# Optimization experiments

Hardware: AMD Instinct MI355X
Metric: run time of the kernel (lower is better)

The kernel has to match this reference:

```python
import jax, jax.numpy as jnp
import numpy as np

H = 32        # num query heads
HKV = 8       # num kv heads
D = 128       # head_dim
SCALE = D ** -0.5
FP8_MAX = 448.0   # e4m3 max
EPS = 1e-8
PAGE = 256
NPAGES = 20
SQ = 1024     # new diffusion tokens
CTX = 3072    # cached context tokens
DIFF_BLK = 32 # diffusion block size


def setup_inputs() -> dict:
    key = jax.random.key(0)
    ks = jax.random.split(key, 6)
    q = jax.random.normal(ks[0], (SQ, H * D), dtype=jnp.float32)
    k = jax.random.normal(ks[1], (SQ, HKV * D), dtype=jnp.float32)
    v = jax.random.normal(ks[2], (SQ, HKV * D), dtype=jnp.float32)
    # paged caches (values already stored in quantized units)
    k_cache = jax.random.normal(ks[3], (NPAGES, PAGE, HKV, D), dtype=jnp.float32)
    v_cache = jax.random.normal(ks[4], (NPAGES, PAGE, HKV, D), dtype=jnp.float32)
    # new tokens go into slots right after the context
    slot_mapping = jnp.arange(CTX, CTX + SQ, dtype=jnp.int32)
    cache_slots = jnp.arange(CTX, dtype=jnp.int32)
    # diffusion mask: full visibility of context, block-causal among new tokens
    blk = jnp.arange(SQ) // DIFF_BLK
    ctx_mask = jnp.ones((SQ, CTX), dtype=bool)
    new_mask = blk[:, None] >= blk[None, :]
    block_mask = jnp.concatenate([ctx_mask, new_mask], axis=1)  # [SQ, CTX+SQ]
    return {"q": q, "k": k, "v": v, "k_cache": k_cache, "v_cache": v_cache,
            "slot_mapping": slot_mapping, "cache_slots": cache_slots,
            "block_mask": block_mask}


def reference(q, k, v, k_cache, v_cache, slot_mapping, cache_slots, block_mask):
    k3 = k.reshape(-1, HKV, D)
    v3 = v.reshape(-1, HKV, D)
    qh = q.reshape(-1, H, D)

    # ---- FP8 scale tracking: per-kv-head absmax over (token, dim) ----
    k_scale = jnp.maximum(jnp.max(jnp.abs(k3), axis=(0, 2)) / FP8_MAX, EPS)  # [HKV]
    v_scale = jnp.maximum(jnp.max(jnp.abs(v3), axis=(0, 2)) / FP8_MAX, EPS)

    # ---- paged KV-cache store with inline quantization ----
    kc = k_cache.reshape(-1, HKV, D)  # [NPAGES*PAGE, HKV, D]
    vc = v_cache.reshape(-1, HKV, D)
    k_q = jnp.clip(k3 / k_scale[None, :, None], -FP8_MAX, FP8_MAX)
    v_q = jnp.clip(v3 / v_scale[None, :, None], -FP8_MAX, FP8_MAX)
    kc = kc.at[slot_mapping].set(k_q)
    vc = vc.at[slot_mapping].set(v_q)

    # ---- load context tokens from cache and dequantize ----
    k_ctx = kc[cache_slots] * k_scale[None, :, None]  # [CTX, HKV, D]
    v_ctx = vc[cache_slots] * v_scale[None, :, None]
    k_comb = jnp.concatenate([k_ctx, k3], axis=0)  # [SKV, HKV, D]
    v_comb = jnp.concatenate([v_ctx, v3], axis=0)

    # ---- GQA flex attention with token-level block mask ----
    G = H // HKV
    k_g = jnp.repeat(k_comb, G, axis=1)  # [SKV, H, D]
    v_g = jnp.repeat(v_comb, G, axis=1)
    scores = jnp.einsum('qhd,khd->hqk', qh, k_g) * SCALE  # [H, SQ, SKV]
    scores = jnp.where(block_mask[None, :, :], scores, jnp.float32(-1e30))
    probs = jax.nn.softmax(scores, axis=-1)
    o = jnp.einsum('hqk,khd->qhd', probs, v_g)  # [SQ, H, D]
    return o.reshape(-1, H * D)
```

## Files before the change

kernel.cpp:

```cpp
#include <hip/hip_runtime.h>
#include <stdint.h>

#define H 32
#define HKV 8
#define D 128
#define SQ 1024
#define CTX 3072
#define SKV 4096
#define FP8_MAX_C 448.0f
#define EPS_C 1e-8f

typedef __attribute__((ext_vector_type(4))) float f32x4;
typedef __attribute__((ext_vector_type(8))) __bf16 bf16x8;
typedef __attribute__((ext_vector_type(8))) unsigned short u16x8;
typedef __attribute__((ext_vector_type(4))) unsigned short u16x4;

__device__ __forceinline__ unsigned short f2bf(float x) {
  unsigned int u = __builtin_bit_cast(unsigned int, x);
  u += 0x7fffu + ((u >> 16) & 1u);
  return (unsigned short)(u >> 16);
}

__device__ __forceinline__ f32x4 mfma16(bf16x8 a, bf16x8 b, f32x4 c) {
  return __builtin_amdgcn_mfma_f32_16x16x32_bf16(a, b, c, 0, 0, 0);
}

__device__ __forceinline__ void gld16(const unsigned short* g, char* l) {
  __builtin_amdgcn_global_load_lds(
      (const __attribute__((address_space(1))) unsigned int*)g,
      (__attribute__((address_space(3))) unsigned int*)l, 16, 0, 0);
}

__device__ __forceinline__ void stage_sync() {
  asm volatile("s_waitcnt vmcnt(0)" ::: "memory");
  __builtin_amdgcn_sched_barrier(0);
  __syncthreads();
}

__global__ void scales_part(const float* __restrict__ k,
                            const float* __restrict__ v,
                            unsigned int* __restrict__ smax) {
  const int b = blockIdx.x & 15;
  const int part = blockIdx.x >> 4;
  const float* src = (b < HKV) ? k : v;
  const int h = b & 7;
  const int tid = threadIdx.x;
  const int d0 = (tid & 31) * 4;
  float mx = 0.f;
  const int t1 = part * 128 + 128;
  for (int t = part * 128 + (tid >> 5); t < t1; t += 8) {
    float4 vv = *reinterpret_cast<const float4*>(src + (size_t)t * (HKV * D) + h * D + d0);
    mx = fmaxf(mx, fmaxf(fmaxf(fabsf(vv.x), fabsf(vv.y)),
                         fmaxf(fabsf(vv.z), fabsf(vv.w))));
  }
  __shared__ float red[256];
  red[tid] = mx;
  __syncthreads();
  for (int s = 128; s > 0; s >>= 1) {
    if (tid < s) red[tid] = fmaxf(red[tid], red[tid + s]);
    __syncthreads();
  }
  if (tid == 0) atomicMax(&smax[b], __float_as_uint(red[0]));
}

__global__ void scales_fin(const unsigned int* __restrict__ smax,
                           float* __restrict__ scales) {
  const int i = threadIdx.x;
  if (i < 16) scales[i] = fmaxf(__uint_as_float(smax[i]) / FP8_MAX_C, EPS_C);
}

__global__ void prep_k(const float* __restrict__ k,
                       const float* __restrict__ k_cache,
                       const int* __restrict__ cache_slots,
                       const float* __restrict__ scales,
                       unsigned short* __restrict__ k_comb) {
  const int tid = blockIdx.x * 256 + threadIdx.x;
  const int d8 = tid & 15;
  const int t = (tid >> 4) & (SKV - 1);
  const int h = tid >> 16;
  const int d0 = d8 * 8;
  const float* src;
  float mul;
  if (t < CTX) {
    int slot = cache_slots[t];
    src = k_cache + (size_t)slot * (HKV * D) + h * D + d0;
    mul = scales[h];
  } else {
    src = k + (size_t)(t - CTX) * (HKV * D) + h * D + d0;
    mul = 1.f;
  }
  float4 a = *reinterpret_cast<const float4*>(src);
  float4 bb = *reinterpret_cast<const float4*>(src + 4);
  u16x8 r;
  r[0] = f2bf(a.x * mul);  r[1] = f2bf(a.y * mul);
  r[2] = f2bf(a.z * mul);  r[3] = f2bf(a.w * mul);
  r[4] = f2bf(bb.x * mul); r[5] = f2bf(bb.y * mul);
  r[6] = f2bf(bb.z * mul); r[7] = f2bf(bb.w * mul);
  *reinterpret_cast<u16x8*>(k_comb + ((size_t)h * SKV + t) * D + d0) = r;
}

__global__ void prep_v(const float* __restrict__ v,
                       const float* __restrict__ v_cache,
                       const int* __restrict__ cache_slots,
                       const float* __restrict__ scales,
                       unsigned short* __restrict__ v_combT) {
  const int tid = blockIdx.x * 256 + threadIdx.x;
  const int d = tid & 127;
  const int t8 = (tid >> 7) & 511;
  const int h = tid >> 16;
  const int t0 = t8 * 8;
  const float sc = scales[8 + h];
  u16x8 r;
#pragma unroll
  for (int i = 0; i < 8; ++i) {
    int t = t0 + i;
    float val;
    if (t < CTX) {
      int slot = cache_slots[t];
      val = v_cache[(size_t)slot * (HKV * D) + h * D + d] * sc;
    } else {
      val = v[(size_t)(t - CTX) * (HKV * D) + h * D + d];
    }
    r[i] = f2bf(val);
  }
  *reinterpret_cast<u16x8*>(v_combT + ((size_t)h * D + d) * SKV + t0) = r;
}

#define LDBF(p) (*reinterpret_cast<const bf16x8*>(p))
#define Z4 ((f32x4){0.f, 0.f, 0.f, 0.f})

#define STAGE(TB, BUFO)                                                        \
  {                                                                            \
    _Pragma("unroll")                                                          \
    for (int j = 0; j < 4; ++j) {                                              \
      const int c = wid * 256 + j * 64 + l;                                    \
      const int r_ = c >> 4;                                                   \
      const int lc_ = (c & 15) ^ (r_ & 7);                                     \
      gld16(kb + (size_t)((TB) + r_) * D + lc_ * 8,                            \
            smem + (BUFO) + (wid * 256 + j * 64) * 16);                        \
      const int dv_ = c >> 3;                                                  \
      const int lv_ = (c & 7) ^ (dv_ & 7);                                     \
      gld16(vb + (size_t)dv_ * SKV + (TB) + lv_ * 8,                           \
            smem + (BUFO) + 16384 + (wid * 256 + j * 64) * 16);                \
    }                                                                          \
  }

#define PK(SREG, PKREG)                                                        \
  {                                                                            \
    float p0_ = __builtin_amdgcn_exp2f(SREG[0] - m);                           \
    float p1_ = __builtin_amdgcn_exp2f(SREG[1] - m);                           \
    float p2_ = __builtin_amdgcn_exp2f(SREG[2] - m);                           \
    float p3_ = __builtin_amdgcn_exp2f(SREG[3] - m);                           \
    rs += (p0_ + p1_) + (p2_ + p3_);                                           \
    PKREG[0] = f2bf(p0_); PKREG[1] = f2bf(p1_);                                \
    PKREG[2] = f2bf(p2_); PKREG[3] = f2bf(p3_);                                \
  }

__launch_bounds__(256, 2)
__global__ void attn_kernel(const float* __restrict__ q,
                            const unsigned short* __restrict__ k_comb,
                            const unsigned short* __restrict__ v_combT,
                            float* __restrict__ out) {
  extern __shared__ __align__(16) char smem[];
  const int bid = blockIdx.x;
  const int hkv = bid & 7;
  const int qt = bid >> 3;
  const int wid = threadIdx.x >> 6;
  const int l = threadIdx.x & 63;
  const int lo = l & 15;
  const int g = l >> 4;
  const int hq = hkv * 4 + wid;
  const int qbase = qt * 16;
  const int nt32 = 97 + (qt >> 1);
  const int n64 = (nt32 + 1) >> 1;
  const bool odd = (nt32 & 1) != 0;

  const unsigned short* kb = k_comb + (size_t)hkv * SKV * D;
  const unsigned short* vb = v_combT + (size_t)hkv * D * SKV;

  bf16x8 qf0, qf1, qf2, qf3;
  {
    const float qs = 0.088388347648318447f * 1.4426950408889634f;
    const float* qp = q + (size_t)(qbase + lo) * (H * D) + hq * D;
#define QLOAD(KS, DST)                                                         \
    {                                                                          \
      float4 a = *reinterpret_cast<const float4*>(qp + KS * 32 + g * 8);       \
      float4 b = *reinterpret_cast<const float4*>(qp + KS * 32 + g * 8 + 4);   \
      union { unsigned short u[8]; bf16x8 v; } f;                              \
      f.u[0] = f2bf(a.x * qs); f.u[1] = f2bf(a.y * qs);                        \
      f.u[2] = f2bf(a.z * qs); f.u[3] = f2bf(a.w * qs);                        \
      f.u[4] = f2bf(b.x * qs); f.u[5] = f2bf(b.y * qs);                        \
      f.u[6] = f2bf(b.z * qs); f.u[7] = f2bf(b.w * qs);                        \
      DST = f.v;                                                               \
    }
    QLOAD(0, qf0) QLOAD(1, qf1) QLOAD(2, qf2) QLOAD(3, qf3)
#undef QLOAD
  }

  f32x4 acc0 = Z4, acc1 = Z4, acc2 = Z4, acc3 = Z4;
  f32x4 acc4 = Z4, acc5 = Z4, acc6 = Z4, acc7 = Z4;
  float m = -1e30f;
  float lsum = 0.f;

  const int xr = lo & 7;
  const int kx0 = ((0 + g) ^ xr) << 4;
  const int kx1 = ((4 + g) ^ xr) << 4;
  const int kx2 = ((8 + g) ^ xr) << 4;
  const int kx3 = ((12 + g) ^ xr) << 4;
  const int vxa = ((g) ^ xr) << 4;
  const int vxb = ((g + 4) ^ xr) << 4;
  const char* kbl = smem + lo * 256;
  const char* vbl = smem + 16384 + lo * 128;
  unsigned short* p_lds = (unsigned short*)(smem + 65536);
  unsigned short* prow = p_lds + (wid * 16 + lo) * 72;

  int cur = 0;
  STAGE(0, 0)
  stage_sync();

  for (int t = 0; t < n64; ++t) {
    const int tb = t * 64;
    if (t + 1 < n64) STAGE(tb + 64, (cur ^ 1) * 32768)

    const char* kc = kbl + cur * 32768;
    const char* vc = vbl + cur * 32768;

    f32x4 s0 = Z4, s1 = Z4, s2 = Z4, s3 = Z4;
    {
      bf16x8 a0 = LDBF(kc + 0 * 4096 + kx0);
      bf16x8 a1 = LDBF(kc + 0 * 4096 + kx1);
      bf16x8 a2 = LDBF(kc + 0 * 4096 + kx2);
      bf16x8 a3 = LDBF(kc + 0 * 4096 + kx3);
      s0 = mfma16(a0, qf0, s0); s0 = mfma16(a1, qf1, s0);
      s0 = mfma16(a2, qf2, s0); s0 = mfma16(a3, qf3, s0);
    }
    {
      bf16x8 a0 = LDBF(kc + 1 * 4096 + kx0);
      bf16x8 a1 = LDBF(kc + 1 * 4096 + kx1);
      bf16x8 a2 = LDBF(kc + 1 * 4096 + kx2);
      bf16x8 a3 = LDBF(kc + 1 * 4096 + kx3);
      s1 = mfma16(a0, qf0, s1); s1 = mfma16(a1, qf1, s1);
      s1 = mfma16(a2, qf2, s1); s1 = mfma16(a3, qf3, s1);
    }
    {
      bf16x8 a0 = LDBF(kc + 2 * 4096 + kx0);
      bf16x8 a1 = LDBF(kc + 2 * 4096 + kx1);
      bf16x8 a2 = LDBF(kc + 2 * 4096 + kx2);
      bf16x8 a3 = LDBF(kc + 2 * 4096 + kx3);
      s2 = mfma16(a0, qf0, s2); s2 = mfma16(a1, qf1, s2);
      s2 = mfma16(a2, qf2, s2); s2 = mfma16(a3, qf3, s2);
    }
    {
      bf16x8 a0 = LDBF(kc + 3 * 4096 + kx0);
      bf16x8 a1 = LDBF(kc + 3 * 4096 + kx1);
      bf16x8 a2 = LDBF(kc + 3 * 4096 + kx2);
      bf16x8 a3 = LDBF(kc + 3 * 4096 + kx3);
      s3 = mfma16(a0, qf0, s3); s3 = mfma16(a1, qf1, s3);
      s3 = mfma16(a2, qf2, s3); s3 = mfma16(a3, qf3, s3);
    }

    if (odd && t == n64 - 1) {
      s2 = (f32x4){-1e30f, -1e30f, -1e30f, -1e30f};
      s3 = (f32x4){-1e30f, -1e30f, -1e30f, -1e30f};
    }

    float pmax = fmaxf(fmaxf(fmaxf(s0[0], s0[1]), fmaxf(s0[2], s0[3])),
                       fmaxf(fmaxf(s1[0], s1[1]), fmaxf(s1[2], s1[3])));
    pmax = fmaxf(pmax,
                 fmaxf(fmaxf(fmaxf(s2[0], s2[1]), fmaxf(s2[2], s2[3])),
                       fmaxf(fmaxf(s3[0], s3[1]), fmaxf(s3[2], s3[3]))));
    if (!__all(pmax - m <= 8.f)) {
      float rm = fmaxf(pmax, __shfl_xor(pmax, 16));
      rm = fmaxf(rm, __shfl_xor(rm, 32));
      float mn = fmaxf(m, rm);
      float scl = __builtin_amdgcn_exp2f(m - mn);
      lsum *= scl;
      acc0 *= scl; acc1 *= scl; acc2 *= scl; acc3 *= scl;
      acc4 *= scl; acc5 *= scl; acc6 *= scl; acc7 *= scl;
      m = mn;
    }

    float rs = 0.f;
    u16x4 pk0, pk1, pk2, pk3;
    PK(s0, pk0) PK(s1, pk1) PK(s2, pk2) PK(s3, pk3)
    lsum += rs;

    *reinterpret_cast<u16x4*>(prow + 0 * 16 + g * 4) = pk0;
    *reinterpret_cast<u16x4*>(prow + 1 * 16 + g * 4) = pk1;
    *reinterpret_cast<u16x4*>(prow + 2 * 16 + g * 4) = pk2;
    *reinterpret_cast<u16x4*>(prow + 3 * 16 + g * 4) = pk3;
    bf16x8 pf0 = LDBF(prow + g * 8);
    bf16x8 pf1 = LDBF(prow + 32 + g * 8);

    {
      bf16x8 va = LDBF(vc + 0 * 2048 + vxa), vb_ = LDBF(vc + 0 * 2048 + vxb);
      acc0 = mfma16(pf0, va, acc0); acc0 = mfma16(pf1, vb_, acc0);
    }
    {
      bf16x8 va = LDBF(vc + 1 * 2048 + vxa), vb_ = LDBF(vc + 1 * 2048 + vxb);
      acc1 = mfma16(pf0, va, acc1); acc1 = mfma16(pf1, vb_, acc1);
    }
    {
      bf16x8 va = LDBF(vc + 2 * 2048 + vxa), vb_ = LDBF(vc + 2 * 2048 + vxb);
      acc2 = mfma16(pf0, va, acc2); acc2 = mfma16(pf1, vb_, acc2);
    }
    {
      bf16x8 va = LDBF(vc + 3 * 2048 + vxa), vb_ = LDBF(vc + 3 * 2048 + vxb);
      acc3 = mfma16(pf0, va, acc3); acc3 = mfma16(pf1, vb_, acc3);
    }
    {
      bf16x8 va = LDBF(vc + 4 * 2048 + vxa), vb_ = LDBF(vc + 4 * 2048 + vxb);
      acc4 = mfma16(pf0, va, acc4); acc4 = mfma16(pf1, vb_, acc4);
    }
    {
      bf16x8 va = LDBF(vc + 5 * 2048 + vxa), vb_ = LDBF(vc + 5 * 2048 + vxb);
      acc5 = mfma16(pf0, va, acc5); acc5 = mfma16(pf1, vb_, acc5);
    }
    {
      bf16x8 va = LDBF(vc + 6 * 2048 + vxa), vb_ = LDBF(vc + 6 * 2048 + vxb);
      acc6 = mfma16(pf0, va, acc6); acc6 = mfma16(pf1, vb_, acc6);
    }
    {
      bf16x8 va = LDBF(vc + 7 * 2048 + vxa), vb_ = LDBF(vc + 7 * 2048 + vxb);
      acc7 = mfma16(pf0, va, acc7); acc7 = mfma16(pf1, vb_, acc7);
    }

    stage_sync();
    cur ^= 1;
  }

  lsum += __shfl_xor(lsum, 16);
  lsum += __shfl_xor(lsum, 32);
#pragma unroll
  for (int r = 0; r < 4; ++r) {
    int src = (l & 48) | (g * 4 + r);
    float inv = 1.f / __shfl(lsum, src);
    float* op = out + (size_t)(qbase + g * 4 + r) * (H * D) + hq * D + lo;
    op[0 * 16] = acc0[r] * inv;
    op[1 * 16] = acc1[r] * inv;
    op[2 * 16] = acc2[r] * inv;
    op[3 * 16] = acc3[r] * inv;
    op[4 * 16] = acc4[r] * inv;
    op[5 * 16] = acc5[r] * inv;
    op[6 * 16] = acc6[r] * inv;
    op[7 * 16] = acc7[r] * inv;
  }
}

extern "C" void kernel_launch(void* const* d_in, const int* in_sizes, int n_in,
                              void* d_out, int out_size, void* d_ws, size_t ws_size,
                              hipStream_t stream) {
  (void)in_sizes; (void)n_in; (void)out_size; (void)ws_size;
  const float* q = (const float*)d_in[0];
  const float* k = (const float*)d_in[1];
  const float* v = (const float*)d_in[2];
  const float* k_cache = (const float*)d_in[3];
  const float* v_cache = (const float*)d_in[4];
  const int* cache_slots = (const int*)d_in[6];
  float* out = (float*)d_out;

  unsigned int* smax = (unsigned int*)d_ws;
  float* scales = (float*)((char*)d_ws + 64);
  unsigned short* k_comb = (unsigned short*)((char*)d_ws + 256);
  unsigned short* v_combT = k_comb + (size_t)HKV * SKV * D;

  hipMemsetAsync(smax, 0, 64, stream);
  scales_part<<<128, 256, 0, stream>>>(k, v, smax);
  scales_fin<<<1, 64, 0, stream>>>(smax, scales);
  prep_k<<<2048, 256, 0, stream>>>(k, k_cache, cache_slots, scales, k_comb);
  prep_v<<<2048, 256, 0, stream>>>(v, v_cache, cache_slots, scales, v_combT);
  attn_kernel<<<512, 256, 74752, stream>>>(q, k_comb, v_combT, out);
}
```

Measured before the change: 133.6 us.

## Process two query heads per wave to reuse K/V LDS fragments

Each wave now computes attention for two query heads of the same KV group instead of one, so every K and V fragment read from LDS feeds two MFMAs. The block shrinks from 4 waves to 2, and the staging loop is reorganised so 128 threads fill the same shared K/V tiles. The two heads share one running max, which must be taken over both heads' scores. This cuts LDS reads per MFMA but doubles accumulator registers and halves the waves available for latency hiding per CU.

Result: slower. 168.3 us (+26.0%).

```diff
diff --git a/kernel.cpp b/kernel.cpp
--- a/kernel.cpp
+++ b/kernel.cpp
@@ -132,31 +132,51 @@
 #define STAGE(TB, BUFO)                                                        \
   {                                                                            \
     _Pragma("unroll")                                                          \
-    for (int j = 0; j < 4; ++j) {                                              \
-      const int c = wid * 256 + j * 64 + l;                                    \
+    for (int j = 0; j < 8; ++j) {                                              \
+      const int c = j * 128 + tid;                                             \
       const int r_ = c >> 4;                                                   \
       const int lc_ = (c & 15) ^ (r_ & 7);                                     \
       gld16(kb + (size_t)((TB) + r_) * D + lc_ * 8,                            \
-            smem + (BUFO) + (wid * 256 + j * 64) * 16);                        \
+            smem + (BUFO) + c * 16);                                           \
       const int dv_ = c >> 3;                                                  \
       const int lv_ = (c & 7) ^ (dv_ & 7);                                     \
       gld16(vb + (size_t)dv_ * SKV + (TB) + lv_ * 8,                           \
-            smem + (BUFO) + 16384 + (wid * 256 + j * 64) * 16);                \
+            smem + (BUFO) + 16384 + c * 16);                                   \
     }                                                                          \
   }
 
-#define PK(SREG, PKREG)                                                        \
+#define PK(SREG, PKREG, RSV)                                                   \
   {                                                                            \
     float p0_ = __builtin_amdgcn_exp2f(SREG[0] - m);                           \
     float p1_ = __builtin_amdgcn_exp2f(SREG[1] - m);                           \
     float p2_ = __builtin_amdgcn_exp2f(SREG[2] - m);                           \
     float p3_ = __builtin_amdgcn_exp2f(SREG[3] - m);                           \
-    rs += (p0_ + p1_) + (p2_ + p3_);                                           \
+    RSV += (p0_ + p1_) + (p2_ + p3_);                                          \
     PKREG[0] = f2bf(p0_); PKREG[1] = f2bf(p1_);                                \
     PKREG[2] = f2bf(p2_); PKREG[3] = f2bf(p3_);                                \
   }
 
-__launch_bounds__(256, 2)
+#define QKSF(SF, SA, SB)                                                       \
+  {                                                                            \
+    bf16x8 a0 = LDBF(kc + SF * 4096 + kx0);                                    \
+    bf16x8 a1 = LDBF(kc + SF * 4096 + kx1);                                    \
+    bf16x8 a2 = LDBF(kc + SF * 4096 + kx2);                                    \
+    bf16x8 a3 = LDBF(kc + SF * 4096 + kx3);                                    \
+    SA = mfma16(a0, qa0, SA); SA = mfma16(a1, qa1, SA);                        \
+    SA = mfma16(a2, qa2, SA); SA = mfma16(a3, qa3, SA);                        \
+    SB = mfma16(a0, qb0, SB); SB = mfma16(a1, qb1, SB);                        \
+    SB = mfma16(a2, qb2, SB); SB = mfma16(a3, qb3, SB);                        \
+  }
+
+#define PVDT(DT, AA, AB)                                                       \
+  {                                                                            \
+    bf16x8 va = LDBF(vc + DT * 2048 + vxa);                                    \
+    bf16x8 vw = LDBF(vc + DT * 2048 + vxb);                                    \
+    AA = mfma16(pfa0, va, AA); AA = mfma16(pfa1, vw, AA);                      \
+    AB = mfma16(pfb0, va, AB); AB = mfma16(pfb1, vw, AB);                      \
+  }
+
+__launch_bounds__(128, 1)
 __global__ void attn_kernel(const float* __restrict__ q,
                             const unsigned short* __restrict__ k_comb,
                             const unsigned short* __restrict__ v_combT,
@@ -165,11 +185,12 @@
   const int bid = blockIdx.x;
   const int hkv = bid & 7;
   const int qt = bid >> 3;
-  const int wid = threadIdx.x >> 6;
-  const int l = threadIdx.x & 63;
+  const int tid = threadIdx.x;
+  const int wid = tid >> 6;
+  const int l = tid & 63;
   const int lo = l & 15;
   const int g = l >> 4;
-  const int hq = hkv * 4 + wid;
+  const int hqa = hkv * 4 + wid * 2;
   const int qbase = qt * 16;
   const int nt32 = 97 + (qt >> 1);
   const int n64 = (nt32 + 1) >> 1;
@@ -178,14 +199,14 @@
   const unsigned short* kb = k_comb + (size_t)hkv * SKV * D;
   const unsigned short* vb = v_combT + (size_t)hkv * D * SKV;
 
-  bf16x8 qf0, qf1, qf2, qf3;
+  bf16x8 qa0, qa1, qa2, qa3, qb0, qb1, qb2, qb3;
   {
     const float qs = 0.088388347648318447f * 1.4426950408889634f;
-    const float* qp = q + (size_t)(qbase + lo) * (H * D) + hq * D;
-#define QLOAD(KS, DST)                                                         \
+    const float* qpA = q + (size_t)(qbase + lo) * (H * D) + hqa * D;
+#define QLOAD(PTR, KS, DST)                                                    \
     {                                                                          \
-      float4 a = *reinterpret_cast<const float4*>(qp + KS * 32 + g * 8);       \
-      float4 b = *reinterpret_cast<const float4*>(qp + KS * 32 + g * 8 + 4);   \
+      float4 a = *reinterpret_cast<const float4*>((PTR) + KS * 32 + g * 8);    \
+      float4 b = *reinterpret_cast<const float4*>((PTR) + KS * 32 + g * 8 + 4);\
       union { unsigned short u[8]; bf16x8 v; } f;                              \
       f.u[0] = f2bf(a.x * qs); f.u[1] = f2bf(a.y * qs);                        \
       f.u[2] = f2bf(a.z * qs); f.u[3] = f2bf(a.w * qs);                        \
@@ -193,14 +214,18 @@
       f.u[6] = f2bf(b.z * qs); f.u[7] = f2bf(b.w * qs);                        \
       DST = f.v;                                                               \
     }
-    QLOAD(0, qf0) QLOAD(1, qf1) QLOAD(2, qf2) QLOAD(3, qf3)
+    QLOAD(qpA, 0, qa0) QLOAD(qpA, 1, qa1) QLOAD(qpA, 2, qa2) QLOAD(qpA, 3, qa3)
+    const float* qpB = qpA + D;
+    QLOAD(qpB, 0, qb0) QLOAD(qpB, 1, qb1) QLOAD(qpB, 2, qb2) QLOAD(qpB, 3, qb3)
 #undef QLOAD
   }
 
-  f32x4 acc0 = Z4, acc1 = Z4, acc2 = Z4, acc3 = Z4;
-  f32x4 acc4 = Z4, acc5 = Z4, acc6 = Z4, acc7 = Z4;
+  f32x4 aa0 = Z4, aa1 = Z4, aa2 = Z4, aa3 = Z4;
+  f32x4 aa4 = Z4, aa5 = Z4, aa6 = Z4, aa7 = Z4;
+  f32x4 ab0 = Z4, ab1 = Z4, ab2 = Z4, ab3 = Z4;
+  f32x4 ab4 = Z4, ab5 = Z4, ab6 = Z4, ab7 = Z4;
   float m = -1e30f;
-  float lsum = 0.f;
+  float lsa = 0.f, lsb = 0.f;
 
   const int xr = lo & 7;
   const int kx0 = ((0 + g) ^ xr) << 4;
@@ -211,8 +236,8 @@
   const int vxb = ((g + 4) ^ xr) << 4;
   const char* kbl = smem + lo * 256;
   const char* vbl = smem + 16384 + lo * 128;
-  unsigned short* p_lds = (unsigned short*)(smem + 65536);
-  unsigned short* prow = p_lds + (wid * 16 + lo) * 72;
+  unsigned short* pra = (unsigned short*)(smem + 65536) + ((wid * 2 + 0) * 16 + lo) * 80;
+  unsigned short* prb = (unsigned short*)(smem + 65536) + ((wid * 2 + 1) * 16 + lo) * 80;
 
   int cur = 0;
   STAGE(0, 0)
@@ -225,125 +250,91 @@
     const char* kc = kbl + cur * 32768;
     const char* vc = vbl + cur * 32768;
 
-    f32x4 s0 = Z4, s1 = Z4, s2 = Z4, s3 = Z4;
-    {
-      bf16x8 a0 = LDBF(kc + 0 * 4096 + kx0);
-      bf16x8 a1 = LDBF(kc + 0 * 4096 + kx1);
-      bf16x8 a2 = LDBF(kc + 0 * 4096 + kx2);
-      bf16x8 a3 = LDBF(kc + 0 * 4096 + kx3);
-      s0 = mfma16(a0, qf0, s0); s0 = mfma16(a1, qf1, s0);
-      s0 = mfma16(a2, qf2, s0); s0 = mfma16(a3, qf3, s0);
+    f32x4 sa0 = Z4, sa1 = Z4, sa2 = Z4, sa3 = Z4;
+    f32x4 sb0 = Z4, sb1 = Z4, sb2 = Z4, sb3 = Z4;
+    QKSF(0, sa0, sb0)
+    QKSF(1, sa1, sb1)
+    QKSF(2, sa2, sb2)
+    QKSF(3, sa3, sb3)
+
+    if (odd && t == n64 - 1) {
+      sa2 = (f32x4){-1e30f, -1e30f, -1e30f, -1e30f};
+      sa3 = (f32x4){-1e30f, -1e30f, -1e30f, -1e30f};
+      sb2 = (f32x4){-1e30f, -1e30f, -1e30f, -1e30f};
+      sb3 = (f32x4){-1e30f, -1e30f, -1e30f, -1e30f};
     }
-    {
-      bf16x8 a0 = LDBF(kc + 1 * 4096 + kx0);
-      bf16x8 a1 = LDBF(kc + 1 * 4096 + kx1);
-      bf16x8 a2 = LDBF(kc + 1 * 4096 + kx2);
-      bf16x8 a3 = LDBF(kc + 1 * 4096 + kx3);
-      s1 = mfma16(a0, qf0, s1); s1 = mfma16(a1, qf1, s1);
-      s1 = mfma16(a2, qf2, s1); s1 = mfma16(a3, qf3, s1);
-    }
-    {
-      bf16x8 a0 = LDBF(kc + 2 * 4096 + kx0);
-      bf16x8 a1 = LDBF(kc + 2 * 4096 + kx1);
-      bf16x8 a2 = LDBF(kc + 2 * 4096 + kx2);
-      bf16x8 a3 = LDBF(kc + 2 * 4096 + kx3);
-      s2 = mfma16(a0, qf0, s2); s2 = mfma16(a1, qf1, s2);
-      s2 = mfma16(a2, qf2, s2); s2 = mfma16(a3, qf3, s2);
-    }
-    {
-      bf16x8 a0 = LDBF(kc + 3 * 4096 + kx0);
-      bf16x8 a1 = LDBF(kc + 3 * 4096 + kx1);
-      bf16x8 a2 = LDBF(kc + 3 * 4096 + kx2);
-      bf16x8 a3 = LDBF(kc + 3 * 4096 + kx3);
-      s3 = mfma16(a0, qf0, s3); s3 = mfma16(a1, qf1, s3);
-      s3 = mfma16(a2, qf2, s3); s3 = mfma16(a3, qf3, s3);
-    }
-
-    if (odd && t == n64 - 1) {
-      s2 = (f32x4){-1e30f, -1e30f, -1e30f, -1e30f};
-      s3 = (f32x4){-1e30f, -1e30f, -1e30f, -1e30f};
-    }
-
-    float pmax = fmaxf(fmaxf(fmaxf(s0[0], s0[1]), fmaxf(s0[2], s0[3])),
-                       fmaxf(fmaxf(s1[0], s1[1]), fmaxf(s1[2], s1[3])));
+
+    float pmax = fmaxf(fmaxf(fmaxf(sa0[0], sa0[1]), fmaxf(sa0[2], sa0[3])),
+                       fmaxf(fmaxf(sa1[0], sa1[1]), fmaxf(sa1[2], sa1[3])));
     pmax = fmaxf(pmax,
-                 fmaxf(fmaxf(fmaxf(s2[0], s2[1]), fmaxf(s2[2], s2[3])),
-                       fmaxf(fmaxf(s3[0], s3[1]), fmaxf(s3[2], s3[3]))));
+                 fmaxf(fmaxf(fmaxf(sa2[0], sa2[1]), fmaxf(sa2[2], sa2[3])),
+                       fmaxf(fmaxf(sa3[0], sa3[1]), fmaxf(sa3[2], sa3[3]))));
+    pmax = fmaxf(pmax,
+                 fmaxf(fmaxf(fmaxf(sb0[0], sb0[1]), fmaxf(sb0[2], sb0[3])),
+                       fmaxf(fmaxf(sb1[0], sb1[1]), fmaxf(sb1[2], sb1[3]))));
+    pmax = fmaxf(pmax,
+                 fmaxf(fmaxf(fmaxf(sb2[0], sb2[1]), fmaxf(sb2[2], sb2[3])),
+                       fmaxf(fmaxf(sb3[0], sb3[1]), fmaxf(sb3[2], sb3[3]))));
     if (!__all(pmax - m <= 8.f)) {
       float rm = fmaxf(pmax, __shfl_xor(pmax, 16));
       rm = fmaxf(rm, __shfl_xor(rm, 32));
       float mn = fmaxf(m, rm);
       float scl = __builtin_amdgcn_exp2f(m - mn);
-      lsum *= scl;
-      acc0 *= scl; acc1 *= scl; acc2 *= scl; acc3 *= scl;
-      acc4 *= scl; acc5 *= scl; acc6 *= scl; acc7 *= scl;
+      lsa *= scl; lsb *= scl;
+      aa0 *= scl; aa1 *= scl; aa2 *= scl; aa3 *= scl;
+      aa4 *= scl; aa5 *= scl; aa6 *= scl; aa7 *= scl;
+      ab0 *= scl; ab1 *= scl; ab2 *= scl; ab3 *= scl;
+      ab4 *= scl; ab5 *= scl; ab6 *= scl; ab7 *= scl;
       m = mn;
     }
 
-    float rs = 0.f;
-    u16x4 pk0, pk1, pk2, pk3;
-    PK(s0, pk0) PK(s1, pk1) PK(s2, pk2) PK(s3, pk3)
-    lsum += rs;
-
-    *reinterpret_cast<u16x4*>(prow + 0 * 16 + g * 4) = pk0;
-    *reinterpret_cast<u16x4*>(prow + 1 * 16 + g * 4) = pk1;
-    *reinterpret_cast<u16x4*>(prow + 2 * 16 + g * 4) = pk2;
-    *reinterpret_cast<u16x4*>(prow + 3 * 16 + g * 4) = pk3;
-    bf16x8 pf0 = LDBF(prow + g * 8);
-    bf16x8 pf1 = LDBF(prow + 32 + g * 8);
-
-    {
-      bf16x8 va = LDBF(vc + 0 * 2048 + vxa), vb_ = LDBF(vc + 0 * 2048 + vxb);
-      acc0 = mfma16(pf0, va, acc0); acc0 = mfma16(pf1, vb_, acc0);
-    }
-    {
-      bf16x8 va = LDBF(vc + 1 * 2048 + vxa), vb_ = LDBF(vc + 1 * 2048 + vxb);
-      acc1 = mfma16(pf0, va, acc1); acc1 = mfma16(pf1, vb_, acc1);
-    }
-    {
-      bf16x8 va = LDBF(vc + 2 * 2048 + vxa), vb_ = LDBF(vc + 2 * 2048 + vxb);
-      acc2 = mfma16(pf0, va, acc2); acc2 = mfma16(pf1, vb_, acc2);
-    }
-    {
-      bf16x8 va = LDBF(vc + 3 * 2048 + vxa), vb_ = LDBF(vc + 3 * 2048 + vxb);
-      acc3 = mfma16(pf0, va, acc3); acc3 = mfma16(pf1, vb_, acc3);
-    }
-    {
-      bf16x8 va = LDBF(vc + 4 * 2048 + vxa), vb_ = LDBF(vc + 4 * 2048 + vxb);
-      acc4 = mfma16(pf0, va, acc4); acc4 = mfma16(pf1, vb_, acc4);
-    }
-    {
-      bf16x8 va = LDBF(vc + 5 * 2048 + vxa), vb_ = LDBF(vc + 5 * 2048 + vxb);
-      acc5 = mfma16(pf0, va, acc5); acc5 = mfma16(pf1, vb_, acc5);
-    }
-    {
-      bf16x8 va = LDBF(vc + 6 * 2048 + vxa), vb_ = LDBF(vc + 6 * 2048 + vxb);
-      acc6 = mfma16(pf0, va, acc6); acc6 = mfma16(pf1, vb_, acc6);
-    }
-    {
-      bf16x8 va = LDBF(vc + 7 * 2048 + vxa), vb_ = LDBF(vc + 7 * 2048 + vxb);
-      acc7 = mfma16(pf0, va, acc7); acc7 = mfma16(pf1, vb_, acc7);
-    }
+    u16x4 ka0, ka1, ka2, ka3, kb0, kb1, kb2, kb3;
+    PK(sa0, ka0, lsa) PK(sa1, ka1, lsa) PK(sa2, ka2, lsa) PK(sa3, ka3, lsa)
+    PK(sb0, kb0, lsb) PK(sb1, kb1, lsb) PK(sb2, kb2, lsb) PK(sb3, kb3, lsb)
+
+    *reinterpret_cast<u16x4*>(pra + 0 * 16 + g * 4) = ka0;
+    *reinterpret_cast<u16x4*>(pra + 1 * 16 + g * 4) = ka1;
+    *reinterpret_cast<u16x4*>(pra + 2 * 16 + g * 4) = ka2;
+    *reinterpret_cast<u16x4*>(pra + 3 * 16 + g * 4) = ka3;
+    *reinterpret_cast<u16x4*>(prb + 0 * 16 + g * 4) = kb0;
+    *reinterpret_cast<u16x4*>(prb + 1 * 16 + g * 4) = kb1;
+    *reinterpret_cast<u16x4*>(prb + 2 * 16 + g * 4) = kb2;
+    *reinterpret_cast<u16x4*>(prb + 3 * 16 + g * 4) = kb3;
+    bf16x8 pfa0 = LDBF(pra + g * 8);
+    bf16x8 pfa1 = LDBF(pra + 32 + g * 8);
+    bf16x8 pfb0 = LDBF(prb + g * 8);
+    bf16x8 pfb1 = LDBF(prb + 32 + g * 8);
+
+    PVDT(0, aa0, ab0)
+    PVDT(1, aa1, ab1)
+    PVDT(2, aa2, ab2)
+    PVDT(3, aa3, ab3)
+    PVDT(4, aa4, ab4)
+    PVDT(5, aa5, ab5)
+    PVDT(6, aa6, ab6)
+    PVDT(7, aa7, ab7)
 
     stage_sync();
     cur ^= 1;
   }
 
-  lsum += __shfl_xor(lsum, 16);
-  lsum += __shfl_xor(lsum, 32);
+  lsa += __shfl_xor(lsa, 16); lsa += __shfl_xor(lsa, 32);
+  lsb += __shfl_xor(lsb, 16); lsb += __shfl_xor(lsb, 32);
 #pragma unroll
   for (int r = 0; r < 4; ++r) {
     int src = (l & 48) | (g * 4 + r);
-    float inv = 1.f / __shfl(lsum, src);
-    float* op = out + (size_t)(qbase + g * 4 + r) * (H * D) + hq * D + lo;
-    op[0 * 16] = acc0[r] * inv;
-    op[1 * 16] = acc1[r] * inv;
-    op[2 * 16] = acc2[r] * inv;
-    op[3 * 16] = acc3[r] * inv;
-    op[4 * 16] = acc4[r] * inv;
-    op[5 * 16] = acc5[r] * inv;
-    op[6 * 16] = acc6[r] * inv;
-    op[7 * 16] = acc7[r] * inv;
+    float inva = 1.f / __shfl(lsa, src);
+    float invb = 1.f / __shfl(lsb, src);
+    float* opa = out + (size_t)(qbase + g * 4 + r) * (H * D) + hqa * D + lo;
+    float* opb = opa + D;
+    opa[0 * 16] = aa0[r] * inva; opb[0 * 16] = ab0[r] * invb;
+    opa[1 * 16] = aa1[r] * inva; opb[1 * 16] = ab1[r] * invb;
+    opa[2 * 16] = aa2[r] * inva; opb[2 * 16] = ab2[r] * invb;
+    opa[3 * 16] = aa3[r] * inva; opb[3 * 16] = ab3[r] * invb;
+    opa[4 * 16] = aa4[r] * inva; opb[4 * 16] = ab4[r] * invb;
+    opa[5 * 16] = aa5[r] * inva; opb[5 * 16] = ab5[r] * invb;
+    opa[6 * 16] = aa6[r] * inva; opb[6 * 16] = ab6[r] * invb;
+    opa[7 * 16] = aa7[r] * inva; opb[7 * 16] = ab7[r] * invb;
   }
 }
 
@@ -369,5 +360,5 @@
   scales_fin<<<1, 64, 0, stream>>>(smax, scales);
   prep_k<<<2048, 256, 0, stream>>>(k, k_cache, cache_slots, scales, k_comb);
   prep_v<<<2048, 256, 0, stream>>>(v, v_cache, cache_slots, scales, v_combT);
-  attn_kernel<<<512, 256, 74752, stream>>>(q, k_comb, v_combT, out);
-}
+  attn_kernel<<<512, 128, 75776, stream>>>(q, k_comb, v_combT, out);
+}
```
